# Performance work log

Measured on AMD Instinct MI355X. Metric: run time of the kernel, lower is better.

## Reference

```python
import jax, jax.numpy as jnp
import numpy as np

D_MODEL = 1024
N_HEAD = 16
N_KV_HEAD = 4
D_K = D_MODEL // N_HEAD          # 64
N_REP = N_HEAD // N_KV_HEAD      # 4
B, S = 2, 2048


def setup_inputs() -> dict:
    key = jax.random.key(0)
    ks = jax.random.split(key, 7)
    scale = 1.0 / np.sqrt(D_MODEL)
    return {
        "q": jax.random.normal(ks[0], (B, S, D_MODEL), jnp.float32),
        "k": jax.random.normal(ks[1], (B, S, D_MODEL), jnp.float32),
        "v": jax.random.normal(ks[2], (B, S, D_MODEL), jnp.float32),
        # weights stored [in, out] (nn.Linear applies x @ W.T; we fold the transpose)
        "W_q": jax.random.normal(ks[3], (D_MODEL, N_HEAD * D_K), jnp.float32) * scale,
        "W_k": jax.random.normal(ks[4], (D_MODEL, N_KV_HEAD * D_K), jnp.float32) * scale,
        "W_v": jax.random.normal(ks[5], (D_MODEL, N_KV_HEAD * D_K), jnp.float32) * scale,
        "W_o": jax.random.normal(ks[6], (D_MODEL, D_MODEL), jnp.float32) * scale,
    }


def reference(q, k, v, W_q, W_k, W_v, W_o):
    batch, seq_q, _ = q.shape
    seq_k = k.shape[1]
    # projections -> [b, h, s, d]
    Q = (q @ W_q).reshape(batch, seq_q, N_HEAD, D_K).transpose(0, 2, 1, 3)
    K = (k @ W_k).reshape(batch, seq_k, N_KV_HEAD, D_K).transpose(0, 2, 1, 3)
    V = (v @ W_v).reshape(batch, seq_k, N_KV_HEAD, D_K).transpose(0, 2, 1, 3)
    # repeat each KV head n_rep times consecutively (matches expand+reshape)
    K = jnp.repeat(K, N_REP, axis=1)  # [b, n_head, seq_k, d_k]
    V = jnp.repeat(V, N_REP, axis=1)
    scores = jnp.einsum('bhqd,bhkd->bhqk', Q, K) / np.sqrt(D_K).astype(jnp.float32)
    attn = jax.nn.softmax(scores, axis=-1)
    out = jnp.einsum('bhqk,bhkd->bhqd', attn, V)  # [b, h, seq_q, d_k]
    out = out.transpose(0, 2, 1, 3).reshape(batch, seq_q, D_MODEL)
    return out @ W_o
```

## Files before the change

kernel.cpp:

```cpp
#include <hip/hip_runtime.h>
#include <hip/hip_bf16.h>
#include <stdint.h>

#define DEVINL __device__ __forceinline__

typedef unsigned short u16;
typedef __bf16 bf16x8 __attribute__((ext_vector_type(8)));
typedef float f32x4 __attribute__((ext_vector_type(4)));
typedef float f32x16 __attribute__((ext_vector_type(16)));
typedef unsigned short u16x8 __attribute__((ext_vector_type(8)));
typedef unsigned int u32x4 __attribute__((ext_vector_type(4)));

constexpr int BATCH = 2, SEQ = 2048, DM = 1024, NH = 16, NKVH = 4, DK = 64;
#define QSCALE 0.18033688f

DEVINL u16 f2bf(float f) {
    unsigned u = __builtin_bit_cast(unsigned, f);
    u += 0x7fffu + ((u >> 16) & 1u);
    return (u16)(u >> 16);
}

DEVINL unsigned pkbf(float a, float b) {
    unsigned r;
    asm("v_cvt_pk_bf16_f32 %0, %1, %2" : "=v"(r) : "v"(a), "v"(b));
    return r;
}
DEVINL void swap32(unsigned& a, unsigned& b) {
    asm("v_permlane32_swap_b32 %0, %1" : "+v"(a), "+v"(b));
}
DEVINL float fexp2(float x) {
    float r;
    asm("v_exp_f32 %0, %1" : "=v"(r) : "v"(x));
    return r;
}

DEVINL void gload16(const void* g, void* l) {
    __builtin_amdgcn_global_load_lds(
        (const __attribute__((address_space(1))) unsigned int*)g,
        (__attribute__((address_space(3))) unsigned int*)l, 16, 0, 0);
}

DEVINL bf16x8 ldfrag(const u16* p) { return *reinterpret_cast<const bf16x8*>(p); }

__global__ __launch_bounds__(256) void prep_kernel(
    const float* __restrict__ q, const float* __restrict__ k, const float* __restrict__ v,
    const float* __restrict__ Wq, const float* __restrict__ Wk,
    const float* __restrict__ Wv, const float* __restrict__ Wo,
    u16* __restrict__ qb, u16* __restrict__ kb, u16* __restrict__ vb,
    u16* __restrict__ Wqt, u16* __restrict__ Wkt,
    u16* __restrict__ Wvt, u16* __restrict__ Wot) {
    __shared__ float tile[32][33];
    int bid = blockIdx.x;
    if (bid < 6144) {
        const float* in;
        u16* out;
        switch (bid >> 11) {
            case 0: in = q; out = qb; break;
            case 1: in = k; out = kb; break;
            default: in = v; out = vb; break;
        }
        int i = (bid & 2047) * 256 + threadIdx.x;
        const float4* p = reinterpret_cast<const float4*>(in) + (size_t)i * 2;
        float4 a = p[0], b = p[1];
        u16x8 o;
        o[0] = f2bf(a.x); o[1] = f2bf(a.y); o[2] = f2bf(a.z); o[3] = f2bf(a.w);
        o[4] = f2bf(b.x); o[5] = f2bf(b.y); o[6] = f2bf(b.z); o[7] = f2bf(b.w);
        reinterpret_cast<u16x8*>(out)[i] = o;
    } else {
        int tb = bid - 6144;
        int z = tb >> 10, rem = tb & 1023;
        const float* W;
        u16* Wt;
        int N;
        switch (z) {
            case 0: W = Wq; Wt = Wqt; N = 1024; break;
            case 1: W = Wk; Wt = Wkt; N = 256; break;
            case 2: W = Wv; Wt = Wvt; N = 256; break;
            default: W = Wo; Wt = Wot; N = 1024; break;
        }
        int n0 = (rem & 31) * 32;
        if (n0 >= N) return;
        int k0 = (rem >> 5) * 32;
        int tx = threadIdx.x & 31, ty = threadIdx.x >> 5;
#pragma unroll
        for (int r = 0; r < 4; ++r)
            tile[ty + 8 * r][tx] = W[(size_t)(k0 + ty + 8 * r) * N + n0 + tx];
        __syncthreads();
#pragma unroll
        for (int r = 0; r < 4; ++r)
            Wt[(size_t)(n0 + ty + 8 * r) * 1024 + k0 + tx] = f2bf(tile[tx][ty + 8 * r]);
    }
}

#define GEMM_CORE64(Apt, Bpt)                                                 \
    __shared__ __align__(16) u16 Al[2][128 * 32];                             \
    __shared__ __align__(16) u16 Bl[2][64 * 32];                              \
    const int tid = threadIdx.x;                                              \
    const int lane = tid & 63;                                                \
    const int w = tid >> 6;                                                   \
    const u16* Ab = (Apt) + (size_t)m0 * 1024;                                \
    const u16* Bb = (Bpt) + (size_t)n0 * 1024;                                \
    f32x4 acc[2][4] = {};                                                     \
    auto stage = [&](int buf, int kt) {                                       \
        const u16* Ag = Ab + kt * 32;                                         \
        const u16* Bg = Bb + kt * 32;                                         \
        _Pragma("unroll") for (int rnd = 0; rnd < 2; ++rnd) {                 \
            int L = tid * 16 + rnd * 4096;                                    \
            int row = L >> 6;                                                 \
            int cb = (L & 63) ^ (((row >> 1) & 3) << 4);                      \
            gload16(Ag + (size_t)row * 1024 + (cb >> 1), &Al[buf][L >> 1]);   \
        }                                                                     \
        {                                                                     \
            int L = tid * 16;                                                 \
            int row = L >> 6;                                                 \
            int cb = (L & 63) ^ (((row >> 1) & 3) << 4);                      \
            gload16(Bg + (size_t)row * 1024 + (cb >> 1), &Bl[buf][L >> 1]);   \
        }                                                                     \
    };                                                                        \
    stage(0, 0);                                                              \
    __syncthreads();                                                          \
    int buf = 0;                                                              \
    for (int kt = 0; kt < 32; ++kt) {                                         \
        if (kt + 1 < 32) stage(buf ^ 1, kt + 1);                              \
        bf16x8 af[2], bfr[4];                                                 \
        _Pragma("unroll") for (int mi = 0; mi < 2; ++mi) {                    \
            int row = w * 32 + mi * 16 + (lane & 15);                         \
            int cb = ((lane >> 4) * 16) ^ (((row >> 1) & 3) << 4);            \
            af[mi] = ldfrag(&Al[buf][row * 32 + (cb >> 1)]);                  \
        }                                                                     \
        _Pragma("unroll") for (int ni = 0; ni < 4; ++ni) {                    \
            int row = ni * 16 + (lane & 15);                                  \
            int cb = ((lane >> 4) * 16) ^ (((row >> 1) & 3) << 4);            \
            bfr[ni] = ldfrag(&Bl[buf][row * 32 + (cb >> 1)]);                 \
        }                                                                     \
        _Pragma("unroll") for (int mi = 0; mi < 2; ++mi)                      \
            _Pragma("unroll") for (int ni = 0; ni < 4; ++ni)                  \
                acc[mi][ni] = __builtin_amdgcn_mfma_f32_16x16x32_bf16(        \
                    af[mi], bfr[ni], acc[mi][ni], 0, 0, 0);                   \
        __syncthreads();                                                      \
        buf ^= 1;                                                             \
    }

__global__ __launch_bounds__(256) void proj_kernel(
    const u16* __restrict__ qb, const u16* __restrict__ kb, const u16* __restrict__ vb,
    const u16* __restrict__ Wqt, const u16* __restrict__ Wkt, const u16* __restrict__ Wvt,
    u16* __restrict__ Qp, u16* __restrict__ Kf, u16* __restrict__ Vf) {
    int bid = blockIdx.x;
    int tile = (bid & 7) * 96 + (bid >> 3);
    const u16 *A, *Bt;
    int m0, n0, z;
    if (tile < 512) {
        z = 0; A = qb; Bt = Wqt; m0 = (tile >> 4) * 128; n0 = (tile & 15) * 64;
    } else if (tile < 640) {
        int t = tile - 512;
        z = 1; A = kb; Bt = Wkt; m0 = (t >> 2) * 128; n0 = (t & 3) * 64;
    } else {
        int t = tile - 640;
        z = 2; A = vb; Bt = Wvt; m0 = (t >> 2) * 128; n0 = (t & 3) * 64;
    }

    GEMM_CORE64(A, Bt)

#pragma unroll
    for (int mi = 0; mi < 2; ++mi)
#pragma unroll
        for (int ni = 0; ni < 4; ++ni)
#pragma unroll
            for (int r = 0; r < 4; ++r) {
                int row = m0 + w * 32 + mi * 16 + (lane >> 4) * 4 + r;
                int col = n0 + ni * 16 + (lane & 15);
                float v = acc[mi][ni][r];
                int bb = row >> 11, s = row & 2047;
                int hh = col >> 6, dd = col & 63;
                if (z == 0) {
                    Qp[((((size_t)bb * NH + hh) * 2048 + s) << 6) + dd] = f2bf(v * QSCALE);
                } else if (z == 1) {
                    size_t base = (size_t)(bb * NKVH + hh) * 131072;
                    int s32 = s >> 5, q31s = s & 31;
                    int c = dd >> 4, hib = (dd >> 3) & 1, j = dd & 7;
                    Kf[base + (size_t)((s32 * 4 + c) * 64 + hib * 32 + q31s) * 8 + j] = f2bf(v);
                } else {
                    size_t base = (size_t)(bb * NKVH + hh) * 131072;
                    int kt = s >> 6, i = (s >> 4) & 3, hib = (s >> 3) & 1, j = s & 7;
                    int dt = dd >> 5, q31v = dd & 31;
                    Vf[base + (size_t)((((kt * 2 + dt) * 4 + i) * 64) + hib * 32 + q31v) * 8 + j] = f2bf(v);
                }
            }
}

__global__ __launch_bounds__(256) void oproj_kernel(const u16* __restrict__ Oa,
                                                    const u16* __restrict__ Wot,
                                                    float* __restrict__ out) {
    int bid = blockIdx.x;
    int tile = (bid & 7) * 64 + (bid >> 3);
    const int m0 = (tile >> 4) * 128, n0 = (tile & 15) * 64;

    GEMM_CORE64(Oa, Wot)

#pragma unroll
    for (int mi = 0; mi < 2; ++mi)
#pragma unroll
        for (int ni = 0; ni < 4; ++ni)
#pragma unroll
            for (int r = 0; r < 4; ++r) {
                int row = m0 + w * 32 + mi * 16 + (lane >> 4) * 4 + r;
                int col = n0 + ni * 16 + (lane & 15);
                out[(size_t)row * 1024 + col] = acc[mi][ni][r];
            }
}

__global__ __launch_bounds__(256) void attn_kernel(const u16* __restrict__ Qp,
                                                   const u16* __restrict__ Kf,
                                                   const u16* __restrict__ Vf,
                                                   u16* __restrict__ Oa) {
    __shared__ float Lods[2][64][36];
    __shared__ float Lsum[2][64];

    const int tid = threadIdx.x;
    const int lane = tid & 63, w = tid >> 6;
    const int half = w >> 1, sub = w & 1;
    const int hi = lane >> 5, q31 = lane & 31;
    const int qt = blockIdx.x, h = blockIdx.y, b = blockIdx.z;
    const int kvh = h >> 2;
    const int qrow = qt * 64 + sub * 32 + q31;

    const u16* Qb = Qp + ((size_t)((b * NH + h) * SEQ) + qrow) * 64 + hi * 8;
    bf16x8 qf0 = ldfrag(Qb), qf1 = ldfrag(Qb + 16);
    bf16x8 qf2 = ldfrag(Qb + 32), qf3 = ldfrag(Qb + 48);

    const u16* Kb = Kf + (size_t)(b * NKVH + kvh) * 131072 + (size_t)half * 65536 + lane * 8;
    const u16* Vb = Vf + (size_t)(b * NKVH + kvh) * 131072 + (size_t)half * 65536 + lane * 8;

    bf16x8 k0[8], k1[8], vf[8];
#pragma unroll
    for (int r = 0; r < 8; ++r) k0[r] = ldfrag(Kb + (size_t)r * 512);
#pragma unroll
    for (int r = 0; r < 8; ++r) k1[r] = ldfrag(Kb + (size_t)(8 + r) * 512);
#pragma unroll
    for (int r = 0; r < 8; ++r) vf[r] = ldfrag(Vb + (size_t)r * 512);

    f32x16 od0 = {}, od1 = {};
    float lsum = 0.f;
    f32x16 sA0 = {}, sA1 = {}, sB0 = {}, sB1 = {};

    sA0 = __builtin_amdgcn_mfma_f32_32x32x16_bf16(k0[0], qf0, sA0, 0, 0, 0);
    sA0 = __builtin_amdgcn_mfma_f32_32x32x16_bf16(k0[1], qf1, sA0, 0, 0, 0);
    sA0 = __builtin_amdgcn_mfma_f32_32x32x16_bf16(k0[2], qf2, sA0, 0, 0, 0);
    sA0 = __builtin_amdgcn_mfma_f32_32x32x16_bf16(k0[3], qf3, sA0, 0, 0, 0);
    sA1 = __builtin_amdgcn_mfma_f32_32x32x16_bf16(k0[4], qf0, sA1, 0, 0, 0);
    sA1 = __builtin_amdgcn_mfma_f32_32x32x16_bf16(k0[5], qf1, sA1, 0, 0, 0);
    sA1 = __builtin_amdgcn_mfma_f32_32x32x16_bf16(k0[6], qf2, sA1, 0, 0, 0);
    sA1 = __builtin_amdgcn_mfma_f32_32x32x16_bf16(k0[7], qf3, sA1, 0, 0, 0);

#define PACKP(sv, s, outf)                                    \
        {                                                     \
            unsigned x0 = pkbf(sv[8 * s + 0], sv[8 * s + 1]); \
            unsigned x1 = pkbf(sv[8 * s + 2], sv[8 * s + 3]); \
            unsigned y0 = pkbf(sv[8 * s + 4], sv[8 * s + 5]); \
            unsigned y1 = pkbf(sv[8 * s + 6], sv[8 * s + 7]); \
            swap32(x0, y0);                                   \
            swap32(x1, y1);                                   \
            u32x4 tt2 = {x0, x1, y0, y1};                     \
            outf = __builtin_bit_cast(bf16x8, tt2);           \
        }

#define BODY(SC0, SC1, SN0, SN1, KQK, KLD, KIDX, VIDX)                        \
    {                                                                         \
        __builtin_amdgcn_s_setprio(1);                                        \
        SN0 = {};                                                             \
        SN1 = {};                                                             \
        SN0 = __builtin_amdgcn_mfma_f32_32x32x16_bf16(KQK[0], qf0, SN0, 0, 0, 0); \
        SN0 = __builtin_amdgcn_mfma_f32_32x32x16_bf16(KQK[1], qf1, SN0, 0, 0, 0); \
        SN0 = __builtin_amdgcn_mfma_f32_32x32x16_bf16(KQK[2], qf2, SN0, 0, 0, 0); \
        SN0 = __builtin_amdgcn_mfma_f32_32x32x16_bf16(KQK[3], qf3, SN0, 0, 0, 0); \
        SN1 = __builtin_amdgcn_mfma_f32_32x32x16_bf16(KQK[4], qf0, SN1, 0, 0, 0); \
        SN1 = __builtin_amdgcn_mfma_f32_32x32x16_bf16(KQK[5], qf1, SN1, 0, 0, 0); \
        SN1 = __builtin_amdgcn_mfma_f32_32x32x16_bf16(KQK[6], qf2, SN1, 0, 0, 0); \
        SN1 = __builtin_amdgcn_mfma_f32_32x32x16_bf16(KQK[7], qf3, SN1, 0, 0, 0); \
        __builtin_amdgcn_s_setprio(0);                                        \
        _Pragma("unroll") for (int r = 0; r < 8; ++r)                         \
            KLD[r] = ldfrag(Kb + (size_t)((KIDX) * 8 + r) * 512);             \
        _Pragma("unroll") for (int r = 0; r < 16; ++r) {                      \
            SC0[r] = fexp2(SC0[r]);                                           \
            SC1[r] = fexp2(SC1[r]);                                           \
        }                                                                     \
        {                                                                     \
            f32x16 ts = SC0 + SC1;                                            \
            float u0 = (ts[0] + ts[1]) + (ts[2] + ts[3]);                     \
            float u1 = (ts[4] + ts[5]) + (ts[6] + ts[7]);                     \
            float u2 = (ts[8] + ts[9]) + (ts[10] + ts[11]);                   \
            float u3 = (ts[12] + ts[13]) + (ts[14] + ts[15]);                 \
            lsum += (u0 + u1) + (u2 + u3);                                    \
        }                                                                     \
        bf16x8 pa0, pa1, pa2, pa3;                                            \
        PACKP(SC0, 0, pa0)                                                    \
        PACKP(SC0, 1, pa1)                                                    \
        PACKP(SC1, 0, pa2)                                                    \
        PACKP(SC1, 1, pa3)                                                    \
        __builtin_amdgcn_s_setprio(1);                                        \
        od0 = __builtin_amdgcn_mfma_f32_32x32x16_bf16(vf[0], pa0, od0, 0, 0, 0); \
        od0 = __builtin_amdgcn_mfma_f32_32x32x16_bf16(vf[1], pa1, od0, 0, 0, 0); \
        od0 = __builtin_amdgcn_mfma_f32_32x32x16_bf16(vf[2], pa2, od0, 0, 0, 0); \
        od0 = __builtin_amdgcn_mfma_f32_32x32x16_bf16(vf[3], pa3, od0, 0, 0, 0); \
        od1 = __builtin_amdgcn_mfma_f32_32x32x16_bf16(vf[4], pa0, od1, 0, 0, 0); \
        od1 = __builtin_amdgcn_mfma_f32_32x32x16_bf16(vf[5], pa1, od1, 0, 0, 0); \
        od1 = __builtin_amdgcn_mfma_f32_32x32x16_bf16(vf[6], pa2, od1, 0, 0, 0); \
        od1 = __builtin_amdgcn_mfma_f32_32x32x16_bf16(vf[7], pa3, od1, 0, 0, 0); \
        __builtin_amdgcn_s_setprio(0);                                        \
        _Pragma("unroll") for (int r = 0; r < 8; ++r)                         \
            vf[r] = ldfrag(Vb + (size_t)((VIDX) * 8 + r) * 512);              \
    }

    for (int tt = 0; tt < 8; ++tt) {
        int t = tt * 2;
        BODY(sA0, sA1, sB0, sB1, k1, k0, (t + 2) & 15, (t + 1) & 15)
        BODY(sB0, sB1, sA0, sA1, k0, k1, (t + 3) & 15, (t + 2) & 15)
    }
#undef BODY
#undef PACKP

    lsum += __shfl_xor(lsum, 32);

    __syncthreads();
    if (half) {
#pragma unroll
        for (int j = 0; j < 4; ++j) {
            f32x4 c0 = {od0[4 * j], od0[4 * j + 1], od0[4 * j + 2], od0[4 * j + 3]};
            f32x4 c1 = {od1[4 * j], od1[4 * j + 1], od1[4 * j + 2], od1[4 * j + 3]};
            *(f32x4*)&Lods[sub][lane][4 * j] = c0;
            *(f32x4*)&Lods[sub][lane][16 + 4 * j] = c1;
        }
        Lsum[sub][lane] = lsum;
    }
    __syncthreads();
    if (!half) {
#pragma unroll
        for (int j = 0; j < 4; ++j) {
            f32x4 c0 = *(const f32x4*)&Lods[sub][lane][4 * j];
            f32x4 c1 = *(const f32x4*)&Lods[sub][lane][16 + 4 * j];
#pragma unroll
            for (int t = 0; t < 4; ++t) {
                od0[4 * j + t] += c0[t];
                od1[4 * j + t] += c1[t];
            }
        }
        lsum += Lsum[sub][lane];

        float inv = 1.0f / lsum;
        u16* Ob = Oa + ((size_t)(b * SEQ) + qrow) * DM + h * 64;
#pragma unroll
        for (int i = 0; i < 8; ++i) {
            int r = 2 * i;
            int d = (r & 3) + 8 * (r >> 2) + 4 * hi;
            *(unsigned*)(Ob + d) = pkbf(od0[r] * inv, od0[r + 1] * inv);
            *(unsigned*)(Ob + 32 + d) = pkbf(od1[r] * inv, od1[r + 1] * inv);
        }
    }
}

extern "C" void kernel_launch(void* const* d_in, const int* in_sizes, int n_in,
                              void* d_out, int out_size, void* d_ws, size_t ws_size,
                              hipStream_t stream) {
    const float* q  = (const float*)d_in[0];
    const float* k  = (const float*)d_in[1];
    const float* v  = (const float*)d_in[2];
    const float* Wq = (const float*)d_in[3];
    const float* Wk = (const float*)d_in[4];
    const float* Wv = (const float*)d_in[5];
    const float* Wo = (const float*)d_in[6];
    float* out = (float*)d_out;

    char* ws = (char*)d_ws;
    u16* qb  = (u16*)(ws + (size_t)0);
    u16* kb  = (u16*)(ws + ((size_t)8 << 20));
    u16* vb  = (u16*)(ws + ((size_t)16 << 20));
    u16* Wqt = (u16*)(ws + ((size_t)24 << 20));
    u16* Wkt = (u16*)(ws + ((size_t)26 << 20));
    u16* Wvt = (u16*)(ws + ((size_t)27 << 20));
    u16* Wot = (u16*)(ws + ((size_t)28 << 20));
    u16* Qp  = (u16*)(ws + ((size_t)30 << 20));
    u16* Kf  = (u16*)(ws + ((size_t)38 << 20));
    u16* Vf  = (u16*)(ws + ((size_t)40 << 20));
    u16* Oa  = (u16*)(ws + ((size_t)42 << 20));

    prep_kernel<<<10240, 256, 0, stream>>>(q, k, v, Wq, Wk, Wv, Wo,
                                           qb, kb, vb, Wqt, Wkt, Wvt, Wot);

    proj_kernel<<<768, 256, 0, stream>>>(qb, kb, vb, Wqt, Wkt, Wvt,
                                         Qp, Kf, Vf);

    attn_kernel<<<dim3(32, 16, 2), 256, 0, stream>>>(Qp, Kf, Vf, Oa);

    oproj_kernel<<<512, 256, 0, stream>>>(Oa, Wot, out);
}
```

Measured before the change: 115.4 us.

## Stage K/V tiles in shared memory and widen attention blocks to 128 queries

```diff
diff --git a/kernel.cpp b/kernel.cpp
--- a/kernel.cpp
+++ b/kernel.cpp
@@ -213,44 +213,57 @@
                                                    const u16* __restrict__ Kf,
                                                    const u16* __restrict__ Vf,
                                                    u16* __restrict__ Oa) {
-    __shared__ float Lods[2][64][36];
-    __shared__ float Lsum[2][64];
+    __shared__ __align__(16) u16 Kl[4][4096];
+    __shared__ __align__(16) u16 Vl[4][4096];
 
     const int tid = threadIdx.x;
     const int lane = tid & 63, w = tid >> 6;
-    const int half = w >> 1, sub = w & 1;
     const int hi = lane >> 5, q31 = lane & 31;
     const int qt = blockIdx.x, h = blockIdx.y, b = blockIdx.z;
     const int kvh = h >> 2;
-    const int qrow = qt * 64 + sub * 32 + q31;
+    const int qrow = qt * 128 + w * 32 + q31;
 
     const u16* Qb = Qp + ((size_t)((b * NH + h) * SEQ) + qrow) * 64 + hi * 8;
     bf16x8 qf0 = ldfrag(Qb), qf1 = ldfrag(Qb + 16);
     bf16x8 qf2 = ldfrag(Qb + 32), qf3 = ldfrag(Qb + 48);
 
-    const u16* Kb = Kf + (size_t)(b * NKVH + kvh) * 131072 + (size_t)half * 65536 + lane * 8;
-    const u16* Vb = Vf + (size_t)(b * NKVH + kvh) * 131072 + (size_t)half * 65536 + lane * 8;
-
-    bf16x8 k0[8], k1[8], vf[8];
-#pragma unroll
-    for (int r = 0; r < 8; ++r) k0[r] = ldfrag(Kb + (size_t)r * 512);
-#pragma unroll
-    for (int r = 0; r < 8; ++r) k1[r] = ldfrag(Kb + (size_t)(8 + r) * 512);
-#pragma unroll
-    for (int r = 0; r < 8; ++r) vf[r] = ldfrag(Vb + (size_t)r * 512);
+    const u16* KbG = Kf + (size_t)(b * NKVH + kvh) * 131072;
+    const u16* VbG = Vf + (size_t)(b * NKVH + kvh) * 131072;
+
+    auto stageT = [&](int slot, int tile) {
+        const u16* Kg = KbG + (size_t)tile * 4096 + lane * 8;
+        const u16* Vg = VbG + (size_t)tile * 4096 + lane * 8;
+        gload16(Kg + w * 512, &Kl[slot][w * 512]);
+        gload16(Kg + (w + 4) * 512, &Kl[slot][(w + 4) * 512]);
+        gload16(Vg + w * 512, &Vl[slot][w * 512]);
+        gload16(Vg + (w + 4) * 512, &Vl[slot][(w + 4) * 512]);
+    };
 
     f32x16 od0 = {}, od1 = {};
     float lsum = 0.f;
     f32x16 sA0 = {}, sA1 = {}, sB0 = {}, sB1 = {};
-
-    sA0 = __builtin_amdgcn_mfma_f32_32x32x16_bf16(k0[0], qf0, sA0, 0, 0, 0);
-    sA0 = __builtin_amdgcn_mfma_f32_32x32x16_bf16(k0[1], qf1, sA0, 0, 0, 0);
-    sA0 = __builtin_amdgcn_mfma_f32_32x32x16_bf16(k0[2], qf2, sA0, 0, 0, 0);
-    sA0 = __builtin_amdgcn_mfma_f32_32x32x16_bf16(k0[3], qf3, sA0, 0, 0, 0);
-    sA1 = __builtin_amdgcn_mfma_f32_32x32x16_bf16(k0[4], qf0, sA1, 0, 0, 0);
-    sA1 = __builtin_amdgcn_mfma_f32_32x32x16_bf16(k0[5], qf1, sA1, 0, 0, 0);
-    sA1 = __builtin_amdgcn_mfma_f32_32x32x16_bf16(k0[6], qf2, sA1, 0, 0, 0);
-    sA1 = __builtin_amdgcn_mfma_f32_32x32x16_bf16(k0[7], qf3, sA1, 0, 0, 0);
+    bf16x8 kA[8], kB[8], vf[8];
+
+    stageT(0, 0);
+    stageT(1, 1);
+    stageT(2, 2);
+    asm volatile("s_waitcnt vmcnt(0)" ::: "memory");
+    __builtin_amdgcn_s_barrier();
+
+#pragma unroll
+    for (int r = 0; r < 8; ++r) kA[r] = ldfrag(&Kl[0][r * 512 + lane * 8]);
+    sA0 = __builtin_amdgcn_mfma_f32_32x32x16_bf16(kA[0], qf0, sA0, 0, 0, 0);
+    sA0 = __builtin_amdgcn_mfma_f32_32x32x16_bf16(kA[1], qf1, sA0, 0, 0, 0);
+    sA0 = __builtin_amdgcn_mfma_f32_32x32x16_bf16(kA[2], qf2, sA0, 0, 0, 0);
+    sA0 = __builtin_amdgcn_mfma_f32_32x32x16_bf16(kA[3], qf3, sA0, 0, 0, 0);
+    sA1 = __builtin_amdgcn_mfma_f32_32x32x16_bf16(kA[4], qf0, sA1, 0, 0, 0);
+    sA1 = __builtin_amdgcn_mfma_f32_32x32x16_bf16(kA[5], qf1, sA1, 0, 0, 0);
+    sA1 = __builtin_amdgcn_mfma_f32_32x32x16_bf16(kA[6], qf2, sA1, 0, 0, 0);
+    sA1 = __builtin_amdgcn_mfma_f32_32x32x16_bf16(kA[7], qf3, sA1, 0, 0, 0);
+#pragma unroll
+    for (int r = 0; r < 8; ++r) kB[r] = ldfrag(&Kl[1][r * 512 + lane * 8]);
+#pragma unroll
+    for (int r = 0; r < 8; ++r) vf[r] = ldfrag(&Vl[0][r * 512 + lane * 8]);
 
 #define PACKP(sv, s, outf)                                    \
         {                                                     \
@@ -264,7 +277,7 @@
             outf = __builtin_bit_cast(bf16x8, tt2);           \
         }
 
-#define BODY(SC0, SC1, SN0, SN1, KQK, KLD, KIDX, VIDX)                        \
+#define BODY(SC0, SC1, SN0, SN1, KQK, KLD, T)                                 \
     {                                                                         \
         __builtin_amdgcn_s_setprio(1);                                        \
         SN0 = {};                                                             \
@@ -278,8 +291,12 @@
         SN1 = __builtin_amdgcn_mfma_f32_32x32x16_bf16(KQK[6], qf2, SN1, 0, 0, 0); \
         SN1 = __builtin_amdgcn_mfma_f32_32x32x16_bf16(KQK[7], qf3, SN1, 0, 0, 0); \
         __builtin_amdgcn_s_setprio(0);                                        \
-        _Pragma("unroll") for (int r = 0; r < 8; ++r)                         \
-            KLD[r] = ldfrag(Kb + (size_t)((KIDX) * 8 + r) * 512);             \
+        stageT(((T) + 3) & 3, ((T) + 3) & 31);                                \
+        {                                                                     \
+            const u16* Ksl = &Kl[((T) + 2) & 3][lane * 8];                    \
+            _Pragma("unroll") for (int r = 0; r < 8; ++r)                     \
+                KLD[r] = ldfrag(Ksl + r * 512);                               \
+        }                                                                     \
         _Pragma("unroll") for (int r = 0; r < 16; ++r) {                      \
             SC0[r] = fexp2(SC0[r]);                                           \
             SC1[r] = fexp2(SC1[r]);                                           \
@@ -307,54 +324,33 @@
         od1 = __builtin_amdgcn_mfma_f32_32x32x16_bf16(vf[6], pa2, od1, 0, 0, 0); \
         od1 = __builtin_amdgcn_mfma_f32_32x32x16_bf16(vf[7], pa3, od1, 0, 0, 0); \
         __builtin_amdgcn_s_setprio(0);                                        \
-        _Pragma("unroll") for (int r = 0; r < 8; ++r)                         \
-            vf[r] = ldfrag(Vb + (size_t)((VIDX) * 8 + r) * 512);              \
-    }
-
-    for (int tt = 0; tt < 8; ++tt) {
+        {                                                                     \
+            const u16* Vsl = &Vl[((T) + 1) & 3][lane * 8];                    \
+            _Pragma("unroll") for (int r = 0; r < 8; ++r)                     \
+                vf[r] = ldfrag(Vsl + r * 512);                                \
+        }                                                                     \
+        asm volatile("s_waitcnt vmcnt(0)" ::: "memory");                      \
+        __builtin_amdgcn_s_barrier();                                         \
+    }
+
+    for (int tt = 0; tt < 16; ++tt) {
         int t = tt * 2;
-        BODY(sA0, sA1, sB0, sB1, k1, k0, (t + 2) & 15, (t + 1) & 15)
-        BODY(sB0, sB1, sA0, sA1, k0, k1, (t + 3) & 15, (t + 2) & 15)
+        BODY(sA0, sA1, sB0, sB1, kB, kA, t)
+        BODY(sB0, sB1, sA0, sA1, kA, kB, t + 1)
     }
 #undef BODY
 #undef PACKP
 
     lsum += __shfl_xor(lsum, 32);
 
-    __syncthreads();
-    if (half) {
-#pragma unroll
-        for (int j = 0; j < 4; ++j) {
-            f32x4 c0 = {od0[4 * j], od0[4 * j + 1], od0[4 * j + 2], od0[4 * j + 3]};
-            f32x4 c1 = {od1[4 * j], od1[4 * j + 1], od1[4 * j + 2], od1[4 * j + 3]};
-            *(f32x4*)&Lods[sub][lane][4 * j] = c0;
-            *(f32x4*)&Lods[sub][lane][16 + 4 * j] = c1;
-        }
-        Lsum[sub][lane] = lsum;
-    }
-    __syncthreads();
-    if (!half) {
-#pragma unroll
-        for (int j = 0; j < 4; ++j) {
-            f32x4 c0 = *(const f32x4*)&Lods[sub][lane][4 * j];
-            f32x4 c1 = *(const f32x4*)&Lods[sub][lane][16 + 4 * j];
-#pragma unroll
-            for (int t = 0; t < 4; ++t) {
-                od0[4 * j + t] += c0[t];
-                od1[4 * j + t] += c1[t];
-            }
-        }
-        lsum += Lsum[sub][lane];
-
-        float inv = 1.0f / lsum;
-        u16* Ob = Oa + ((size_t)(b * SEQ) + qrow) * DM + h * 64;
-#pragma unroll
-        for (int i = 0; i < 8; ++i) {
-            int r = 2 * i;
-            int d = (r & 3) + 8 * (r >> 2) + 4 * hi;
-            *(unsigned*)(Ob + d) = pkbf(od0[r] * inv, od0[r + 1] * inv);
-            *(unsigned*)(Ob + 32 + d) = pkbf(od1[r] * inv, od1[r + 1] * inv);
-        }
+    float inv = 1.0f / lsum;
+    u16* Ob = Oa + ((size_t)(b * SEQ) + qrow) * DM + h * 64;
+#pragma unroll
+    for (int i = 0; i < 8; ++i) {
+        int r = 2 * i;
+        int d = (r & 3) + 8 * (r >> 2) + 4 * hi;
+        *(unsigned*)(Ob + d) = pkbf(od0[r] * inv, od0[r + 1] * inv);
+        *(unsigned*)(Ob + 32 + d) = pkbf(od1[r] * inv, od1[r + 1] * inv);
     }
 }
 
@@ -389,7 +385,7 @@
     proj_kernel<<<768, 256, 0, stream>>>(qb, kb, vb, Wqt, Wkt, Wvt,
                                          Qp, Kf, Vf);
 
-    attn_kernel<<<dim3(32, 16, 2), 256, 0, stream>>>(Qp, Kf, Vf, Oa);
+    attn_kernel<<<dim3(16, 16, 2), 256, 0, stream>>>(Qp, Kf, Vf, Oa);
 
     oproj_kernel<<<512, 256, 0, stream>>>(Oa, Wot, out);
 }
```

Measured after the change: 113.9 us. Within noise of the previous version (-1.3%).
